# Kernel tuning notes

Hardware: AMD Instinct MI355X
Metric: run time of the kernel (lower is better)

Reference implementation:

```python
import jax, jax.numpy as jnp
import numpy as np

EPS = 1e-08  # smooth in CELoss


def _lovasz_grad(fg_sorted):
    # Alg. 1 of the Lovasz-Softmax paper; fg_sorted: [P] floats in {0,1}
    gts = fg_sorted.sum()
    intersection = gts - jnp.cumsum(fg_sorted)
    union = gts + jnp.cumsum(1.0 - fg_sorted)
    jaccard = 1.0 - intersection / union
    # first-difference: jaccard[1:] - jaccard[:-1], keep jaccard[0]
    return jnp.concatenate([jaccard[:1], jaccard[1:] - jaccard[:-1]])


def setup_inputs() -> dict:
    key = jax.random.key(0)
    k1, k2 = jax.random.split(key)
    B, C, D, H, W = 1, 3, 96, 256, 256
    probas = jax.random.normal(k1, (B, C, D, H, W), dtype=jnp.float32)
    cls = jax.random.randint(k2, (B, D, H, W), 0, C)
    # one-hot label volume [B, C, D, H, W], matching labels[0][c] == 1 usage
    labels = jax.nn.one_hot(cls, C, axis=1, dtype=jnp.int32)
    weight = jnp.ones((C,), dtype=jnp.float32)  # weight=[1,1,1]
    return {"probas": probas, "weight": weight, "labels": labels}


def reference(probas, weight, labels):
    C = probas.shape[1]
    # flatten_probas (dim==5 path): softmax over classes, flatten to [P, C]
    p = jax.nn.softmax(probas, axis=1)
    p = jnp.moveaxis(p, 1, -1).reshape(-1, C)
    # label reconstruction: 0*ch0 + 1*ch1 + 2*ch2 from one-hot channels
    lab = (labels[0, 1] + 2 * labels[0, 2]).reshape(-1)  # [P] int class ids

    total = jnp.zeros((), dtype=p.dtype)
    count = jnp.zeros((), dtype=p.dtype)
    for c in range(C):
        fg = (lab == c).astype(p.dtype)              # [P]
        present = fg.sum() > 0                       # classes='present'
        # CELoss(softmax=False, average='None'): -fg * log(pred + eps)
        errors = -fg * jnp.log(p[:, c] + EPS)        # [P]
        order = jnp.argsort(-errors)                 # descending sort perm
        errors_sorted = errors[order]
        fg_sorted = fg[order]
        g = jax.lax.stop_gradient(_lovasz_grad(fg_sorted))
        loss_c = weight[c] * jnp.dot(errors_sorted, g)
        total = total + jnp.where(present, loss_c, 0.0)
        count = count + jnp.where(present, 1.0, 0.0)
    # mean over present classes (empty -> 0)
    return jnp.where(count > 0, total / jnp.maximum(count, 1.0), 0.0)
```

## Files before the change

kernel.cpp:

```cpp
#include <hip/hip_runtime.h>


#define EPS 1e-8f
#define BLK 256
#define GPT 3
#define GPB (GPT*BLK)

typedef float fx4 __attribute__((ext_vector_type(4)));
typedef int   ix4 __attribute__((ext_vector_type(4)));

__device__ __forceinline__ void px_acc(float za, float zb, float zc, int la, int lb,
                                       float& s0, float& s1, float& s2,
                                       float& n0, float& n1, float& n2)
{
    float m  = fmaxf(za, fmaxf(zb, zc));
    float ea = __expf(za - m);
    float eb = __expf(zb - m);
    float ec = __expf(zc - m);
    float d  = ea + eb + ec;
    float q  = (la != 0) ? eb : ((lb != 0) ? ec : ea);
    float err = __logf(d) - __logf(fmaf(EPS, d, q));
    float f1 = (la != 0) ? 1.f : 0.f;
    float f2 = (lb != 0) ? 1.f : 0.f;
    float f0 = 1.f - f1 - f2;
    s0 += f0 * err;  s1 += f1 * err;  s2 += f2 * err;
    n0 += f0;        n1 += f1;        n2 += f2;
}

__global__ __launch_bounds__(BLK) void lovasz_reduce_kernel(
    const float* __restrict__ probas,
    const int*   __restrict__ labels,
    float* __restrict__ partial,
    int P4, int P, int nfull, int nblocks)
{
    const fx4* z0 = (const fx4*)(probas);
    const fx4* z1 = (const fx4*)(probas + (size_t)P);
    const fx4* z2 = (const fx4*)(probas + 2 * (size_t)P);
    const ix4* l1 = (const ix4*)(labels + (size_t)P);
    const ix4* l2 = (const ix4*)(labels + 2 * (size_t)P);

    float s0 = 0.f, s1 = 0.f, s2 = 0.f;
    float n0 = 0.f, n1 = 0.f, n2 = 0.f;

    const int base = blockIdx.x * GPB + threadIdx.x;

    if (blockIdx.x < nfull) {
        #pragma unroll
        for (int j = 0; j < GPT; ++j) {
            int i = base + j * BLK;
            fx4 a = __builtin_nontemporal_load(&z0[i]);
            fx4 b = __builtin_nontemporal_load(&z1[i]);
            fx4 c = __builtin_nontemporal_load(&z2[i]);
            ix4 u = __builtin_nontemporal_load(&l1[i]);
            ix4 v = __builtin_nontemporal_load(&l2[i]);
            px_acc(a.x, b.x, c.x, u.x, v.x, s0, s1, s2, n0, n1, n2);
            px_acc(a.y, b.y, c.y, u.y, v.y, s0, s1, s2, n0, n1, n2);
            px_acc(a.z, b.z, c.z, u.z, v.z, s0, s1, s2, n0, n1, n2);
            px_acc(a.w, b.w, c.w, u.w, v.w, s0, s1, s2, n0, n1, n2);
        }
    } else {
        #pragma unroll
        for (int j = 0; j < GPT; ++j) {
            int i = base + j * BLK;
            if (i < P4) {
                fx4 a = __builtin_nontemporal_load(&z0[i]);
                fx4 b = __builtin_nontemporal_load(&z1[i]);
                fx4 c = __builtin_nontemporal_load(&z2[i]);
                ix4 u = __builtin_nontemporal_load(&l1[i]);
                ix4 v = __builtin_nontemporal_load(&l2[i]);
                px_acc(a.x, b.x, c.x, u.x, v.x, s0, s1, s2, n0, n1, n2);
                px_acc(a.y, b.y, c.y, u.y, v.y, s0, s1, s2, n0, n1, n2);
                px_acc(a.z, b.z, c.z, u.z, v.z, s0, s1, s2, n0, n1, n2);
                px_acc(a.w, b.w, c.w, u.w, v.w, s0, s1, s2, n0, n1, n2);
            }
        }
    }

    #pragma unroll
    for (int off = 32; off > 0; off >>= 1) {
        s0 += __shfl_down(s0, off);
        s1 += __shfl_down(s1, off);
        s2 += __shfl_down(s2, off);
        n0 += __shfl_down(n0, off);
        n1 += __shfl_down(n1, off);
        n2 += __shfl_down(n2, off);
    }

    __shared__ float red[6][4];
    int wave = threadIdx.x >> 6;
    int lane = threadIdx.x & 63;
    if (lane == 0) {
        red[0][wave] = s0; red[1][wave] = s1; red[2][wave] = s2;
        red[3][wave] = n0; red[4][wave] = n1; red[5][wave] = n2;
    }
    __syncthreads();
    if (threadIdx.x < 6) {
        int k = threadIdx.x;
        partial[(size_t)k * nblocks + blockIdx.x] =
            red[k][0] + red[k][1] + red[k][2] + red[k][3];
    }
}

__global__ __launch_bounds__(256) void lovasz_finalize_kernel(
    const float* __restrict__ partial, int nblocks,
    const float* __restrict__ probas, const int* __restrict__ labels,
    const float* __restrict__ weight, float* __restrict__ out,
    int P4, int P)
{
    float acc[6] = {0.f, 0.f, 0.f, 0.f, 0.f, 0.f};
    for (int b = threadIdx.x; b < nblocks; b += 256) {
        #pragma unroll
        for (int k = 0; k < 6; ++k)
            acc[k] += partial[(size_t)k * nblocks + b];
    }

    #pragma unroll
    for (int k = 0; k < 6; ++k)
        #pragma unroll
        for (int off = 32; off > 0; off >>= 1)
            acc[k] += __shfl_down(acc[k], off);

    __shared__ float red[6][4];
    int wave = threadIdx.x >> 6;
    int lane = threadIdx.x & 63;
    if (lane == 0) {
        #pragma unroll
        for (int k = 0; k < 6; ++k) red[k][wave] = acc[k];
    }
    __syncthreads();
    if (threadIdx.x == 0) {
        float s[6];
        #pragma unroll
        for (int k = 0; k < 6; ++k)
            s[k] = red[k][0] + red[k][1] + red[k][2] + red[k][3];
        for (int i = 4 * P4; i < P; ++i) {
            px_acc(probas[i], probas[(size_t)P + i], probas[2 * (size_t)P + i],
                   labels[(size_t)P + i], labels[2 * (size_t)P + i],
                   s[0], s[1], s[2], s[3], s[4], s[5]);
        }
        float total = 0.f, cnt = 0.f;
        #pragma unroll
        for (int c = 0; c < 3; ++c) {
            if (s[3 + c] > 0.f) {
                total += weight[c] * s[c] / s[3 + c];
                cnt += 1.f;
            }
        }
        out[0] = (cnt > 0.f) ? total / cnt : 0.f;
    }
}

extern "C" void kernel_launch(void* const* d_in, const int* in_sizes, int n_in,
                              void* d_out, int out_size, void* d_ws, size_t ws_size,
                              hipStream_t stream) {
    const float* probas = (const float*)d_in[0];
    const float* weight = (const float*)d_in[1];
    const int*   labels = (const int*)d_in[2];
    float* partial = (float*)d_ws;

    int total = in_sizes[0];
    int P  = total / 3;
    int P4 = P / 4;
    int nfull = P4 / GPB;
    int rem = P4 - nfull * GPB;
    int nblocks = nfull + (rem ? 1 : 0);

    lovasz_reduce_kernel<<<nblocks, BLK, 0, stream>>>(probas, labels, partial,
                                                      P4, P, nfull, nblocks);
    lovasz_finalize_kernel<<<1, 256, 0, stream>>>(partial, nblocks, probas,
                                                  labels, weight, (float*)d_out,
                                                  P4, P);
}
```

Baseline: 155.3 us.

## Stream inputs through LDS with global_load_lds and grid-stride loop

Replaces direct nontemporal vector loads into registers with asynchronous global-to-LDS DMA loads (16 bytes per lane) for the five input streams. Each block then reads its tile back from LDS. The grid is fixed at 2048 blocks iterating in a grid-stride loop, with a separate tail path. The single LDS buffer needs a barrier before and after each load, so loads from different iterations can no longer overlap, which may reduce memory-level parallelism compared with the previous fully unrolled loads.

```diff
diff --git a/kernel.cpp b/kernel.cpp
--- a/kernel.cpp
+++ b/kernel.cpp
@@ -3,11 +3,19 @@
 
 #define EPS 1e-8f
 #define BLK 256
-#define GPT 3
-#define GPB (GPT*BLK)
+#define STREAM_TILE (BLK * 16)
+#define NSTREAM 5
+#define LDS_BYTES (NSTREAM * STREAM_TILE)
 
 typedef float fx4 __attribute__((ext_vector_type(4)));
 typedef int   ix4 __attribute__((ext_vector_type(4)));
+
+__device__ __forceinline__ void dma16(const void* g, void* l) {
+    __builtin_amdgcn_global_load_lds(
+        (const __attribute__((address_space(1))) unsigned int*)g,
+        (__attribute__((address_space(3))) unsigned int*)l,
+        16, 0, 0);
+}
 
 __device__ __forceinline__ void px_acc(float za, float zb, float zc, int la, int lb,
                                        float& s0, float& s1, float& s2,
@@ -31,48 +39,59 @@
     const float* __restrict__ probas,
     const int*   __restrict__ labels,
     float* __restrict__ partial,
-    int P4, int P, int nfull, int nblocks)
+    int P4, int P, int niter, int nblocks)
 {
-    const fx4* z0 = (const fx4*)(probas);
-    const fx4* z1 = (const fx4*)(probas + (size_t)P);
-    const fx4* z2 = (const fx4*)(probas + 2 * (size_t)P);
-    const ix4* l1 = (const ix4*)(labels + (size_t)P);
-    const ix4* l2 = (const ix4*)(labels + 2 * (size_t)P);
+    __shared__ char lds_raw[LDS_BYTES];
+
+    const char* gbase[NSTREAM] = {
+        (const char*)probas,
+        (const char*)(probas + (size_t)P),
+        (const char*)(probas + 2 * (size_t)P),
+        (const char*)(labels + (size_t)P),
+        (const char*)(labels + 2 * (size_t)P)
+    };
 
     float s0 = 0.f, s1 = 0.f, s2 = 0.f;
     float n0 = 0.f, n1 = 0.f, n2 = 0.f;
 
-    const int base = blockIdx.x * GPB + threadIdx.x;
+    const int tid = threadIdx.x;
+    const int wave_lds = (tid & ~63) * 16;
 
-    if (blockIdx.x < nfull) {
+    for (int it = 0; it < niter; ++it) {
+        size_t i = ((size_t)it * nblocks + blockIdx.x) * BLK + tid;
+
+        if (it > 0) __syncthreads();
         #pragma unroll
-        for (int j = 0; j < GPT; ++j) {
-            int i = base + j * BLK;
-            fx4 a = __builtin_nontemporal_load(&z0[i]);
-            fx4 b = __builtin_nontemporal_load(&z1[i]);
-            fx4 c = __builtin_nontemporal_load(&z2[i]);
-            ix4 u = __builtin_nontemporal_load(&l1[i]);
-            ix4 v = __builtin_nontemporal_load(&l2[i]);
+        for (int s = 0; s < NSTREAM; ++s) {
+            dma16(gbase[s] + i * 16, lds_raw + s * STREAM_TILE + wave_lds);
+        }
+        __syncthreads();
+
+        fx4 a = *(const fx4*)(lds_raw + 0 * STREAM_TILE + tid * 16);
+        fx4 b = *(const fx4*)(lds_raw + 1 * STREAM_TILE + tid * 16);
+        fx4 c = *(const fx4*)(lds_raw + 2 * STREAM_TILE + tid * 16);
+        ix4 u = *(const ix4*)(lds_raw + 3 * STREAM_TILE + tid * 16);
+        ix4 v = *(const ix4*)(lds_raw + 4 * STREAM_TILE + tid * 16);
+
+        px_acc(a.x, b.x, c.x, u.x, v.x, s0, s1, s2, n0, n1, n2);
+        px_acc(a.y, b.y, c.y, u.y, v.y, s0, s1, s2, n0, n1, n2);
+        px_acc(a.z, b.z, c.z, u.z, v.z, s0, s1, s2, n0, n1, n2);
+        px_acc(a.w, b.w, c.w, u.w, v.w, s0, s1, s2, n0, n1, n2);
+    }
+
+    {
+        size_t done = (size_t)niter * nblocks * BLK;
+        size_t g = done + (size_t)blockIdx.x * BLK + tid;
+        if (g < (size_t)P4) {
+            fx4 a = *(const fx4*)(gbase[0] + g * 16);
+            fx4 b = *(const fx4*)(gbase[1] + g * 16);
+            fx4 c = *(const fx4*)(gbase[2] + g * 16);
+            ix4 u = *(const ix4*)(gbase[3] + g * 16);
+            ix4 v = *(const ix4*)(gbase[4] + g * 16);
             px_acc(a.x, b.x, c.x, u.x, v.x, s0, s1, s2, n0, n1, n2);
             px_acc(a.y, b.y, c.y, u.y, v.y, s0, s1, s2, n0, n1, n2);
             px_acc(a.z, b.z, c.z, u.z, v.z, s0, s1, s2, n0, n1, n2);
             px_acc(a.w, b.w, c.w, u.w, v.w, s0, s1, s2, n0, n1, n2);
-        }
-    } else {
-        #pragma unroll
-        for (int j = 0; j < GPT; ++j) {
-            int i = base + j * BLK;
-            if (i < P4) {
-                fx4 a = __builtin_nontemporal_load(&z0[i]);
-                fx4 b = __builtin_nontemporal_load(&z1[i]);
-                fx4 c = __builtin_nontemporal_load(&z2[i]);
-                ix4 u = __builtin_nontemporal_load(&l1[i]);
-                ix4 v = __builtin_nontemporal_load(&l2[i]);
-                px_acc(a.x, b.x, c.x, u.x, v.x, s0, s1, s2, n0, n1, n2);
-                px_acc(a.y, b.y, c.y, u.y, v.y, s0, s1, s2, n0, n1, n2);
-                px_acc(a.z, b.z, c.z, u.z, v.z, s0, s1, s2, n0, n1, n2);
-                px_acc(a.w, b.w, c.w, u.w, v.w, s0, s1, s2, n0, n1, n2);
-            }
         }
     }
 
@@ -86,18 +105,19 @@
         n2 += __shfl_down(n2, off);
     }
 
-    __shared__ float red[6][4];
-    int wave = threadIdx.x >> 6;
-    int lane = threadIdx.x & 63;
+    __syncthreads();
+    float* red = (float*)lds_raw;
+    int wave = tid >> 6;
+    int lane = tid & 63;
     if (lane == 0) {
-        red[0][wave] = s0; red[1][wave] = s1; red[2][wave] = s2;
-        red[3][wave] = n0; red[4][wave] = n1; red[5][wave] = n2;
+        red[0 * 4 + wave] = s0; red[1 * 4 + wave] = s1; red[2 * 4 + wave] = s2;
+        red[3 * 4 + wave] = n0; red[4 * 4 + wave] = n1; red[5 * 4 + wave] = n2;
     }
     __syncthreads();
-    if (threadIdx.x < 6) {
-        int k = threadIdx.x;
+    if (tid < 6) {
+        int k = tid;
         partial[(size_t)k * nblocks + blockIdx.x] =
-            red[k][0] + red[k][1] + red[k][2] + red[k][3];
+            red[k * 4 + 0] + red[k * 4 + 1] + red[k * 4 + 2] + red[k * 4 + 3];
     }
 }
 
@@ -161,12 +181,12 @@
     int total = in_sizes[0];
     int P  = total / 3;
     int P4 = P / 4;
-    int nfull = P4 / GPB;
-    int rem = P4 - nfull * GPB;
-    int nblocks = nfull + (rem ? 1 : 0);
+
+    const int nblocks = 2048;
+    int niter = P4 / (nblocks * BLK);
 
     lovasz_reduce_kernel<<<nblocks, BLK, 0, stream>>>(probas, labels, partial,
-                                                      P4, P, nfull, nblocks);
+                                                      P4, P, niter, nblocks);
     lovasz_finalize_kernel<<<1, 256, 0, stream>>>(partial, nblocks, probas,
                                                   labels, weight, (float*)d_out,
                                                   P4, P);
```

Result: slower. 165.4 us (+6.5%).
